# Optimization experiments

Measured on AMD Instinct MI355X. Metric: run time of the kernel, lower is better.

The kernel has to match this reference:

```python
import jax, jax.numpy as jnp
import numpy as np

H = 512      # hidden_size
NH = 4       # num_heads (default)
D = H // NH  # head_dim = 128
B = 2
S = 256
PI = float(np.pi)


def setup_inputs() -> dict:
    key = jax.random.key(0)
    ks = iter(jax.random.split(key, 40))
    n = lambda *s: jax.random.normal(next(ks), s, jnp.float32) * 0.02
    z = lambda *s: jnp.zeros(s, jnp.float32)
    return dict(
        x=jax.random.normal(next(ks), (B, S, H), jnp.float32),
        # WaveInteractionAttention projections (stored as (in,out): y = x @ W + b)
        Wq=n(H, H), bq=z(H), Wk=n(H, H), bk=z(H), Wv=n(H, H), bv=z(H), Wo=n(H, H), bo=z(H),
        # WaveletAttention Conv1d weights, torch layout (O, I, K), kernels 3/5/9
        cw1=n(H, H, 3), cb1=z(H), cw2=n(H, H, 5), cb2=z(H), cw3=n(H, H, 9), cb3=z(H),
        scale_w=jnp.ones((3,), jnp.float32) / 3.0, Wwl=n(H, H), bwl=z(H),
        # PhaseInteractionLayer
        Wtc=n(H, 2 * H), btc=z(2 * H), Wfc=n(2 * H, H), bfc=z(H),
        phase_shifts=jax.random.normal(next(ks), (1, 1, H), jnp.float32) * 0.1,
        # final concat projection + LayerNorm
        Wproj=n(3 * H, H), bproj=z(H), ln_g=jnp.ones((H,), jnp.float32), ln_b=z(H),
    )


def reference(x, Wq, bq, Wk, bk, Wv, bv, Wo, bo,
              cw1, cb1, cw2, cb2, cw3, cb3, scale_w, Wwl, bwl,
              Wtc, btc, Wfc, bfc, phase_shifts, Wproj, bproj, ln_g, ln_b):
    Bs, Sl, Hs = x.shape

    # ---- WaveInteractionAttention ----
    def heads(W, b):  # (B,S,H) -> (B,NH,S,D)
        return jnp.transpose((x @ W + b).reshape(Bs, Sl, NH, D), (0, 2, 1, 3))

    q, k, v = heads(Wq, bq), heads(Wk, bk), heads(Wv, bv)
    omega = jax.nn.sigmoid(q) * PI        # (B,NH,S,D)
    amp = jax.nn.sigmoid(k)
    ph = jnp.tanh(v) * PI
    pos = (jnp.arange(Sl)[:, None] - jnp.arange(Sl)[None, :]).astype(jnp.float32)  # (S,S): i-j
    # scores[b,h,i,j,d] = amp[b,h,i,d] * cos(omega[b,h,i,d]*(i-j) + phase[b,h,i,d])
    scores = amp[:, :, :, None, :] * jnp.cos(
        omega[:, :, :, None, :] * pos[None, None, :, :, None] + ph[:, :, :, None, :])
    patterns = jax.nn.softmax(scores * (1.0 / np.sqrt(D)), axis=3)  # softmax over j
    ctx = jnp.einsum('bhijd,bhjd->bhid', patterns, v)               # (B,NH,S,D)
    wave_out = jnp.transpose(ctx, (0, 2, 1, 3)).reshape(Bs, Sl, Hs) @ Wo + bo

    # ---- WaveletAttention (multi-scale Conv1d; 'same' length) ----
    xc = jnp.transpose(x, (0, 2, 1))  # (B,H,S)

    def conv(w, b, p):
        y = jax.lax.conv_general_dilated(xc, w, (1,), [(p, p)],
                                         dimension_numbers=('NCH', 'OIH', 'NCH'))
        return y + b[None, :, None]

    sw = jax.nn.softmax(scale_w)
    comb = sw[0] * conv(cw1, cb1, 1) + sw[1] * conv(cw2, cb2, 2) + sw[2] * conv(cw3, cb3, 4)
    wavelet_out = jnp.transpose(comb, (0, 2, 1)) @ Wwl + bwl

    # ---- PhaseInteractionLayer ----
    cr = x @ Wtc + btc
    real, imag = cr[..., :Hs], cr[..., Hs:]
    mag = jnp.sqrt(real ** 2 + imag ** 2 + 1e-5)
    p = jnp.arctan2(imag, real)  # (B,S,H)
    # mean_j cos(p_i - p_j + s) == cos(p_i+s)*mean_j cos(p_j) + sin(p_i+s)*mean_j sin(p_j)
    mc = jnp.mean(jnp.cos(p), axis=1, keepdims=True)
    ms = jnp.mean(jnp.sin(p), axis=1, keepdims=True)
    mixed = jnp.cos(p + phase_shifts) * mc + jnp.sin(p + phase_shifts) * ms
    new_p = p + 0.1 * mixed
    nc = jnp.concatenate([mag * jnp.cos(new_p), mag * jnp.sin(new_p)], axis=-1)
    phase_out = nc @ Wfc + bfc

    # ---- combine + residual + LayerNorm (dropout in eval mode = identity) ----
    combined = jnp.concatenate([wave_out, wavelet_out, phase_out], axis=-1) @ Wproj + bproj
    out = x + combined
    mu = jnp.mean(out, axis=-1, keepdims=True)
    var = jnp.mean((out - mu) ** 2, axis=-1, keepdims=True)
    return (out - mu) / jnp.sqrt(var + 1e-5) * ln_g + ln_b
```

## Files before the change

### kernel.cpp

```cpp
#include <hip/hip_runtime.h>
#include <math.h>

#define H 512
#define B 2
#define S 256
#define BS 512
#define PI_F 3.14159265358979323846f
#define INV_SQRT_D 0.08838834764831845f

typedef __attribute__((ext_vector_type(8))) short short8;
typedef __attribute__((ext_vector_type(4))) float f32x4;
typedef __attribute__((ext_vector_type(4))) unsigned short ushort4v;

__device__ __forceinline__ unsigned short f2bf(float f) {
    unsigned u = __float_as_uint(f);
    u += 0x7FFFu + ((u >> 16) & 1u);
    return (unsigned short)(u >> 16);
}
__device__ __forceinline__ float bf2f(unsigned short u) {
    return __uint_as_float((unsigned)u << 16);
}

__device__ __forceinline__ void softmax3(const float* sw, float& w0, float& w1, float& w2)
{
    float s0 = sw[0], s1 = sw[1], s2 = sw[2];
    float mx = fmaxf(s0, fmaxf(s1, s2));
    float e0 = __expf(s0 - mx), e1 = __expf(s1 - mx), e2 = __expf(s2 - mx);
    float inv = 1.f / (e0 + e1 + e2);
    w0 = e0 * inv; w1 = e1 * inv; w2 = e2 * inv;
}

__device__ __forceinline__ void gload16(const unsigned short* g, void* l) {
    __builtin_amdgcn_global_load_lds(
        (const __attribute__((address_space(1))) unsigned int*)g,
        (__attribute__((address_space(3))) unsigned int*)l,
        16, 0, 0);
}

template<int EPI>
__device__ __forceinline__ void gemm_body(
    const unsigned short* __restrict__ Ablk, int lda,
    const unsigned short* __restrict__ Btblk, int ldb,
    const float* __restrict__ bias,
    void* __restrict__ Cout, int ldc,
    int row0, int col0, int nk,
    unsigned short (*As)[4096], unsigned short (*Bs)[4096],
    unsigned short* __restrict__ aux = nullptr)
{
    const int tid = threadIdx.x;
    const int lane = tid & 63, wave = tid >> 6;
    const int wr = wave >> 1, wc = wave & 1;
    const int rowA = tid >> 3;
    const int sb = ((tid & 7) << 4) ^ ((rowA & 7) << 4);
    const size_t offA0 = (size_t)rowA * lda + (sb >> 1);
    const size_t offA1 = offA0 + (size_t)32 * lda;
    const size_t offB0 = (size_t)rowA * ldb + (sb >> 1);
    const size_t offB1 = offB0 + (size_t)32 * ldb;
    const unsigned ldsO0 = wave * 1024u, ldsO1 = ldsO0 + 4096u;

    const int fr = lane & 15, grp = lane >> 4;
    int aA[2][2], aB[2][2];
    #pragma unroll
    for (int kk = 0; kk < 2; ++kk)
        #pragma unroll
        for (int f = 0; f < 2; ++f) {
            int ra = wr * 32 + f * 16 + fr;
            int rb = wc * 32 + f * 16 + fr;
            aA[f][kk] = (ra * 128 + kk * 64 + grp * 16) ^ ((ra & 7) << 4);
            aB[f][kk] = (rb * 128 + kk * 64 + grp * 16) ^ ((rb & 7) << 4);
        }

    auto stage = [&](int buf, int k0) {
        char* ab = (char*)As[buf]; char* bb = (char*)Bs[buf];
        gload16(Ablk  + offA0 + k0, ab + ldsO0);
        gload16(Ablk  + offA1 + k0, ab + ldsO1);
        gload16(Btblk + offB0 + k0, bb + ldsO0);
        gload16(Btblk + offB1 + k0, bb + ldsO1);
    };

    stage(0, 0);
    __syncthreads();
    f32x4 acc[2][2] = {};
    int cur = 0;
    for (int t = 0; t < nk; ++t) {
        if (t + 1 < nk) stage(cur ^ 1, (t + 1) * 64);
        const char* AsB = (const char*)As[cur];
        const char* BsB = (const char*)Bs[cur];
        #pragma unroll
        for (int kk = 0; kk < 2; ++kk) {
            short8 a0 = *(const short8*)(AsB + aA[0][kk]);
            short8 a1 = *(const short8*)(AsB + aA[1][kk]);
            short8 b0 = *(const short8*)(BsB + aB[0][kk]);
            short8 b1 = *(const short8*)(BsB + aB[1][kk]);
            acc[0][0] = __builtin_amdgcn_mfma_f32_16x16x32_bf16(a0, b0, acc[0][0], 0, 0, 0);
            acc[0][1] = __builtin_amdgcn_mfma_f32_16x16x32_bf16(a0, b1, acc[0][1], 0, 0, 0);
            acc[1][0] = __builtin_amdgcn_mfma_f32_16x16x32_bf16(a1, b0, acc[1][0], 0, 0, 0);
            acc[1][1] = __builtin_amdgcn_mfma_f32_16x16x32_bf16(a1, b1, acc[1][1], 0, 0, 0);
        }
        __syncthreads();
        cur ^= 1;
    }

    const int erow = row0 + wr * 32 + grp * 4;
    const int ecol = col0 + wc * 32 + fr;
    #pragma unroll
    for (int fm = 0; fm < 2; ++fm)
        #pragma unroll
        for (int fn = 0; fn < 2; ++fn)
            #pragma unroll
            for (int j = 0; j < 4; ++j) {
                int r = erow + fm * 16 + j;
                int c = ecol + fn * 16;
                float v = acc[fm][fn][j];
                if (EPI == 1) {
                    v += bias[c];
                    if (c < 512)       v = PI_F / (1.f + __expf(-v));
                    else if (c < 1024) v = 1.f  / (1.f + __expf(-v));
                    ((float*)Cout)[(size_t)r * ldc + c] = v;
                    if (c >= 1024 && c < 1536)
                        aux[(size_t)r * 512 + (c - 1024)] = f2bf(v);
                } else if (EPI == 4) {
                    ((unsigned short*)Cout)[(size_t)r * ldc + c] = f2bf(v);
                } else {
                    ((float*)Cout)[(size_t)r * ldc + c] = v;
                }
            }
}

__device__ __forceinline__ void conv_body(
    const unsigned short* __restrict__ xpad,
    const unsigned short* __restrict__ WbigT,
    float* __restrict__ convP, int bm, int bn, int z,
    unsigned short (*As)[4096], unsigned short (*Bs)[4096])
{
    const int tid = threadIdx.x;
    const int lane = tid & 63, wave = tid >> 6;
    const int wr = wave >> 1, wc = wave & 1;
    const int rowA = tid >> 3;
    const int sb = ((tid & 7) << 4) ^ ((rowA & 7) << 4);
    const int sbk = sb >> 1;
    const int r0 = bm * 64 + rowA;
    const int base0 = ((r0 >> 8) * 264 + (r0 & 255)) * 512;
    const int r1 = r0 + 32;
    const int base1 = ((r1 >> 8) * 264 + (r1 & 255)) * 512;
    const size_t offB0 = (size_t)(bn * 64 + rowA) * 4608 + sbk;
    const size_t offB1 = offB0 + (size_t)32 * 4608;
    const unsigned ldsO0 = wave * 1024u, ldsO1 = ldsO0 + 4096u;
    const int kstart = z * 1152;

    const int fr = lane & 15, grp = lane >> 4;
    int aA[2][2], aB[2][2];
    #pragma unroll
    for (int kk = 0; kk < 2; ++kk)
        #pragma unroll
        for (int f = 0; f < 2; ++f) {
            int ra = wr * 32 + f * 16 + fr;
            int rb = wc * 32 + f * 16 + fr;
            aA[f][kk] = (ra * 128 + kk * 64 + grp * 16) ^ ((ra & 7) << 4);
            aB[f][kk] = (rb * 128 + kk * 64 + grp * 16) ^ ((rb & 7) << 4);
        }

    auto stage = [&](int buf, int k0) {
        int tap = k0 >> 9;
        int ro = tap * 512 + (k0 & 511) + sbk;
        char* ab = (char*)As[buf]; char* bb = (char*)Bs[buf];
        gload16(xpad + base0 + ro, ab + ldsO0);
        gload16(xpad + base1 + ro, ab + ldsO1);
        gload16(WbigT + offB0 + k0, bb + ldsO0);
        gload16(WbigT + offB1 + k0, bb + ldsO1);
    };

    stage(0, kstart);
    __syncthreads();
    f32x4 acc[2][2] = {};
    int cur = 0;
    for (int t = 0; t < 18; ++t) {
        if (t < 17) stage(cur ^ 1, kstart + (t + 1) * 64);
        const char* AsB = (const char*)As[cur];
        const char* BsB = (const char*)Bs[cur];
        #pragma unroll
        for (int kk = 0; kk < 2; ++kk) {
            short8 a0 = *(const short8*)(AsB + aA[0][kk]);
            short8 a1 = *(const short8*)(AsB + aA[1][kk]);
            short8 b0 = *(const short8*)(BsB + aB[0][kk]);
            short8 b1 = *(const short8*)(BsB + aB[1][kk]);
            acc[0][0] = __builtin_amdgcn_mfma_f32_16x16x32_bf16(a0, b0, acc[0][0], 0, 0, 0);
            acc[0][1] = __builtin_amdgcn_mfma_f32_16x16x32_bf16(a0, b1, acc[0][1], 0, 0, 0);
            acc[1][0] = __builtin_amdgcn_mfma_f32_16x16x32_bf16(a1, b0, acc[1][0], 0, 0, 0);
            acc[1][1] = __builtin_amdgcn_mfma_f32_16x16x32_bf16(a1, b1, acc[1][1], 0, 0, 0);
        }
        __syncthreads();
        cur ^= 1;
    }

    float* Cp = convP + (size_t)z * 262144;
    const int erow = bm * 64 + wr * 32 + grp * 4;
    const int ecol = bn * 64 + wc * 32 + fr;
    #pragma unroll
    for (int fm = 0; fm < 2; ++fm)
        #pragma unroll
        for (int fn = 0; fn < 2; ++fn)
            #pragma unroll
            for (int j = 0; j < 4; ++j)
                Cp[(size_t)(erow + fm * 16 + j) * 512 + ecol + fn * 16] = acc[fm][fn][j];
}

__global__ __launch_bounds__(256)
void prep_all(const float* __restrict__ x,
              const float* __restrict__ Wq, const float* __restrict__ Wk,
              const float* __restrict__ Wv, const float* __restrict__ Wtc,
              const float* __restrict__ Wo, const float* __restrict__ Wwl,
              const float* __restrict__ Wfc, const float* __restrict__ Wproj,
              const float* __restrict__ cw1, const float* __restrict__ cw2,
              const float* __restrict__ cw3, const float* __restrict__ scale_w,
              const float* __restrict__ bq, const float* __restrict__ bk,
              const float* __restrict__ bv, const float* __restrict__ btc,
              const float* __restrict__ cb1, const float* __restrict__ cb2,
              const float* __restrict__ cb3,
              const float* __restrict__ bo, const float* __restrict__ bwl,
              const float* __restrict__ bfc, const float* __restrict__ phase_shifts,
              unsigned short* __restrict__ xpad, unsigned short* __restrict__ WcatT,
              unsigned short* __restrict__ WbigT, unsigned short* __restrict__ WprojT,
              unsigned short* __restrict__ Wo_b, unsigned short* __restrict__ Wwl_b,
              unsigned short* __restrict__ Wfc_b,
              float* __restrict__ bcat1, float* __restrict__ beff,
              float* __restrict__ cps, float* __restrict__ sps,
              float* __restrict__ bias_effP)
{
    int bid = blockIdx.x, tid = threadIdx.x;

    if (bid < 64) {
        int k0 = bid * 24;
        float a0 = 0.f, a1 = 0.f;
        #pragma unroll
        for (int m = 0; m < 24; ++m) {
            int k = k0 + m;
            float w = (k < 512) ? bo[k] : (k < 1024) ? bwl[k - 512] : bfc[k - 1024];
            a0 = fmaf(w, Wproj[(size_t)k * 512 + tid], a0);
            a1 = fmaf(w, Wproj[(size_t)k * 512 + tid + 256], a1);
        }
        bias_effP[(size_t)bid * 512 + tid] = a0;
        bias_effP[(size_t)bid * 512 + tid + 256] = a1;
        return;
    }
    bid -= 64;
    if (bid < 1024) {
        int oi = bid * 256 + tid;
        int o = oi >> 9, i = oi & 511;
        float w0, w1, w2; softmax3(scale_w, w0, w1, w2);
        float wt[9];
        #pragma unroll
        for (int t = 0; t < 9; ++t) wt[t] = w2 * cw3[(size_t)oi * 9 + t];
        #pragma unroll
        for (int t = 0; t < 3; ++t) wt[t + 3] = fmaf(w0, cw1[(size_t)oi * 3 + t], wt[t + 3]);
        #pragma unroll
        for (int t = 0; t < 5; ++t) wt[t + 2] = fmaf(w1, cw2[(size_t)oi * 5 + t], wt[t + 2]);
        unsigned short* dst = WbigT + (size_t)o * 4608 + i;
        #pragma unroll
        for (int t = 0; t < 9; ++t) dst[t * 512] = f2bf(wt[t]);
        return;
    }
    bid -= 1024;
    if (bid < 2048) {
        __shared__ float tile[32][33];
        int t = bid;
        const float* src; unsigned short* dst;
        int srcld, dstld, ntk, drow0;
        if (t < 256)       {            src = Wq;    srcld = 512;  dst = WcatT;  dstld = 512;  ntk = 16; drow0 = 0; }
        else if (t < 512)  { t -= 256;  src = Wk;    srcld = 512;  dst = WcatT;  dstld = 512;  ntk = 16; drow0 = 512; }
        else if (t < 768)  { t -= 512;  src = Wv;    srcld = 512;  dst = WcatT;  dstld = 512;  ntk = 16; drow0 = 1024; }
        else if (t < 1280) { t -= 768;  src = Wtc;   srcld = 1024; dst = WcatT;  dstld = 512;  ntk = 16; drow0 = 1536; }
        else               { t -= 1280; src = Wproj; srcld = 512;  dst = WprojT; dstld = 1536; ntk = 48; drow0 = 0; }
        int tk = t % ntk, tn = t / ntk;
        int r8 = tid >> 5, c = tid & 31;
        #pragma unroll
        for (int rr = 0; rr < 4; ++rr) {
            int r = r8 + rr * 8;
            tile[r][c] = src[(size_t)(tk * 32 + r) * srcld + tn * 32 + c];
        }
        __syncthreads();
        #pragma unroll
        for (int rr = 0; rr < 4; ++rr) {
            int r = r8 + rr * 8;
            dst[(size_t)(drow0 + tn * 32 + r) * dstld + tk * 32 + c] = f2bf(tile[c][r]);
        }
        return;
    }
    bid -= 2048;
    if (bid < 264) {
        int e = bid * 1024 + tid * 4;
        int b = e / 135168, rem = e - b * 135168;
        int srow = rem >> 9, i4 = rem & 511;
        int s2 = srow - 4;
        ushort4v pk = {0, 0, 0, 0};
        if (s2 >= 0 && s2 < 256) {
            f32x4 v = *(const f32x4*)&x[((size_t)(b * 256 + s2) << 9) + i4];
            pk[0] = f2bf(v[0]); pk[1] = f2bf(v[1]); pk[2] = f2bf(v[2]); pk[3] = f2bf(v[3]);
        }
        *(ushort4v*)&xpad[e] = pk;
        return;
    }
    bid -= 264;
    if (bid < 1024) {
        int f = bid * 1024 + tid * 4;
        const float* src; unsigned short* dst; int o;
        if (f < 262144)      { src = Wo;  dst = Wo_b;  o = f; }
        else if (f < 524288) { src = Wwl; dst = Wwl_b; o = f - 262144; }
        else                 { src = Wfc; dst = Wfc_b; o = f - 524288; }
        f32x4 v = *(const f32x4*)&src[o];
        ushort4v pk;
        pk[0] = f2bf(v[0]); pk[1] = f2bf(v[1]); pk[2] = f2bf(v[2]); pk[3] = f2bf(v[3]);
        *(ushort4v*)&dst[o] = pk;
        return;
    }
    bid -= 1024;
    {
        int idx = bid * 256 + tid;
        if (idx < 2560) {
            float v;
            if (idx < 512)       v = bq[idx];
            else if (idx < 1024) v = bk[idx - 512];
            else if (idx < 1536) v = bv[idx - 1024];
            else                 v = btc[idx - 1536];
            bcat1[idx] = v;
        } else if (idx < 3072) {
            int c = idx - 2560;
            float w0, w1, w2; softmax3(scale_w, w0, w1, w2);
            beff[c] = w0 * cb1[c] + w1 * cb2[c] + w2 * cb3[c];
        } else if (idx < 3584) {
            int c = idx - 3072;
            float sn, cn; sincosf(phase_shifts[c], &sn, &cn);
            cps[c] = cn; sps[c] = sn;
        }
    }
}

__global__ __launch_bounds__(256)
void big_gemms(const unsigned short* __restrict__ xpad,
               const unsigned short* __restrict__ WbigT, float* __restrict__ convP,
               const unsigned short* __restrict__ WcatT, const float* __restrict__ bcat1,
               float* __restrict__ qkvt, unsigned short* __restrict__ vb16,
               const unsigned short* __restrict__ WprojT,
               const unsigned short* __restrict__ Wo_b, const unsigned short* __restrict__ Wwl_b,
               const unsigned short* __restrict__ Wfc_b,
               unsigned short* __restrict__ WeffCat_T)
{
    __shared__ unsigned short As[2][4096], Bs[2][4096];
    int bid = blockIdx.x;
    if (bid < 256) {
        conv_body(xpad, WbigT, convP, (bid >> 3) & 7, bid & 7, bid >> 6, As, Bs);
        return;
    }
    bid -= 256;
    if (bid < 320) {
        int bm = bid / 40, bn = bid % 40;
        int r0 = bm * 64;
        const unsigned short* Axp = xpad + ((size_t)(r0 >> 8) * 264 + (r0 & 255) + 4) * 512;
        gemm_body<1>(Axp, 512, WcatT + (size_t)bn * 64 * 512, 512, bcat1,
                     qkvt, 2560, r0, bn * 64, 8, As, Bs, vb16);
        return;
    }
    bid -= 320;
    if (bid < 64) {
        int bm = bid >> 3, bn = bid & 7;
        gemm_body<4>(WprojT + (size_t)bm * 64 * 1536, 1536, Wo_b + (size_t)bn * 64 * 512, 512,
                     nullptr, WeffCat_T, 2048, bm * 64, bn * 64, 8, As, Bs);
        return;
    }
    bid -= 64;
    if (bid < 64) {
        int bm = bid >> 3, bn = bid & 7;
        gemm_body<4>(WprojT + 512 + (size_t)bm * 64 * 1536, 1536, Wwl_b + (size_t)bn * 64 * 512, 512,
                     nullptr, WeffCat_T + 512, 2048, bm * 64, bn * 64, 8, As, Bs);
        return;
    }
    bid -= 64;
    {
        int bm = bid >> 4, bn = bid & 15;
        gemm_body<4>(WprojT + 1024 + (size_t)bm * 64 * 1536, 1536, Wfc_b + (size_t)bn * 64 * 512, 512,
                     nullptr, WeffCat_T + 1024, 2048, bm * 64, bn * 64, 8, As, Bs);
    }
}

__global__ __launch_bounds__(256)
void branches(const float* __restrict__ qkvt, const unsigned short* __restrict__ vb16,
              const float* __restrict__ cps, const float* __restrict__ sps,
              const float* __restrict__ convP, const float* __restrict__ beff,
              const float* __restrict__ bias_effP, const float* __restrict__ bproj,
              unsigned short* __restrict__ A_cat, float* __restrict__ bias_eff)
{
    int bid = blockIdx.x, tid = threadIdx.x;
    if (bid < 1024) {
        const int bi = bid >> 1;
        const int b = bi >> 8, i = bi & 255;
        const int c = ((bid & 1) << 8) + tid;
        const float* qrow = qkvt + (size_t)bi * 2560;
        const float om = qrow[c];
        const float am = qrow[512 + c] * INV_SQRT_D;
        const float ph = tanhf(qrow[1024 + c]) * PI_F;
        float cosom, sinom, cc, ss;
        sincosf(om, &sinom, &cosom);
        sincosf(fmaf(om, (float)i, ph), &ss, &cc);
        const unsigned short* vb = vb16 + (size_t)(b * 256) * 512 + c;
        float se = 0.f, sev = 0.f;
        #pragma unroll 4
        for (int j = 0; j < 256; ++j) {
            float e = __expf(am * cc);
            se += e;
            sev = fmaf(e, bf2f(vb[(size_t)j * 512]), sev);
            float cn = fmaf(cc, cosom, ss * sinom);
            ss = fmaf(ss, cosom, -cc * sinom);
            cc = cn;
        }
        A_cat[(size_t)bi * 2048 + c] = f2bf(sev / se);
        return;
    }
    bid -= 1024;
    if (bid < 1024) {
        const int b = bid >> 9, c = bid & 511;
        const int s = tid;
        const float* row = qkvt + (size_t)(b * 256 + s) * 2560 + 1536;
        float re = row[c], im = row[c + 512];
        float hyp2 = fmaf(re, re, im * im);
        float mag = sqrtf(hyp2 + 1e-5f);
        float rh = rsqrtf(fmaxf(hyp2, 1e-30f));
        float cp = re * rh, sp = im * rh;
        float cs = cp, sn = sp;
        #pragma unroll
        for (int m = 32; m; m >>= 1) { cs += __shfl_xor(cs, m); sn += __shfl_xor(sn, m); }
        __shared__ float wred[8];
        int w = s >> 6, l = s & 63;
        if (l == 0) { wred[w] = cs; wred[4 + w] = sn; }
        __syncthreads();
        float mcv = (wred[0] + wred[1] + wred[2] + wred[3]) * (1.f / 256.f);
        float msv = (wred[4] + wred[5] + wred[6] + wred[7]) * (1.f / 256.f);
        float cq = cps[c], sq = sps[c];
        float cpps = cp * cq - sp * sq;
        float spps = sp * cq + cp * sq;
        float d = 0.1f * (cpps * mcv + spps * msv);
        float d2 = d * d;
        float cosd = 1.f - d2 * (0.5f - d2 * (1.f / 24.f));
        float sind = d * (1.f - d2 * ((1.f / 6.f) - d2 * (1.f / 120.f)));
        float cnp = cp * cosd - sp * sind;
        float snp = sp * cosd + cp * sind;
        size_t o = (size_t)(b * 256 + s) * 2048 + c;
        A_cat[o + 1024] = f2bf(mag * cnp);
        A_cat[o + 1536] = f2bf(mag * snp);
        return;
    }
    bid -= 1024;
    if (bid < 1024) {
        int idx = bid * 256 + tid;
        int r = idx >> 9, c = idx & 511;
        float v = beff[c] + convP[idx] + convP[idx + 262144] + convP[idx + 524288] + convP[idx + 786432];
        A_cat[(size_t)r * 2048 + 512 + c] = f2bf(v);
        return;
    }
    bid -= 1024;
    {
        int j = bid * 256 + tid;
        float acc = bproj[j];
        #pragma unroll
        for (int p = 0; p < 64; ++p) acc += bias_effP[(size_t)p * 512 + j];
        bias_eff[j] = acc;
    }
}

__global__ __launch_bounds__(256)
void mid_gemm(const unsigned short* __restrict__ A_cat,
              const unsigned short* __restrict__ WeffCat_T,
              float* __restrict__ P)
{
    __shared__ unsigned short As[2][4096], Bs[2][4096];
    int bid = blockIdx.x;
    int z = bid >> 6, bm = (bid >> 3) & 7, bn = bid & 7;
    gemm_body<3>(A_cat + (size_t)bm * 64 * 2048 + z * 512, 2048,
                 WeffCat_T + (size_t)bn * 64 * 2048 + z * 512, 2048,
                 nullptr, P + (size_t)z * 262144, 512, bm * 64, bn * 64, 8, As, Bs);
}

__global__ __launch_bounds__(256)
void final_ln(const float* __restrict__ x, const float* __restrict__ P,
              const float* __restrict__ bias_eff,
              const float* __restrict__ g, const float* __restrict__ bta,
              float* __restrict__ out)
{
    int r = blockIdx.x, t = threadIdx.x;
    size_t o0 = (size_t)r * 512 + t, o1 = o0 + 256;
    float c0 = bias_eff[t]       + P[o0] + P[o0 + 262144] + P[o0 + 524288] + P[o0 + 786432];
    float c1 = bias_eff[t + 256] + P[o1] + P[o1 + 262144] + P[o1 + 524288] + P[o1 + 786432];
    float v0 = x[o0] + c0, v1 = x[o1] + c1;
    float sum = v0 + v1;
    #pragma unroll
    for (int m = 32; m; m >>= 1) sum += __shfl_xor(sum, m);
    __shared__ float wred[8];
    int w = t >> 6, l = t & 63;
    if (l == 0) wred[w] = sum;
    __syncthreads();
    float mu = (wred[0] + wred[1] + wred[2] + wred[3]) * (1.f / 512.f);
    float d0 = v0 - mu, d1 = v1 - mu;
    float s2 = d0 * d0 + d1 * d1;
    #pragma unroll
    for (int m = 32; m; m >>= 1) s2 += __shfl_xor(s2, m);
    if (l == 0) wred[4 + w] = s2;
    __syncthreads();
    float inv = rsqrtf((wred[4] + wred[5] + wred[6] + wred[7]) * (1.f / 512.f) + 1e-5f);
    out[o0] = d0 * inv * g[t]       + bta[t];
    out[o1] = d1 * inv * g[t + 256] + bta[t + 256];
}

extern "C" void kernel_launch(void* const* d_in, const int* in_sizes, int n_in,
                              void* d_out, int out_size, void* d_ws, size_t ws_size,
                              hipStream_t stream)
{
    const float* x   = (const float*)d_in[0];
    const float* Wq  = (const float*)d_in[1];
    const float* bq  = (const float*)d_in[2];
    const float* Wk  = (const float*)d_in[3];
    const float* bk  = (const float*)d_in[4];
    const float* Wv  = (const float*)d_in[5];
    const float* bv  = (const float*)d_in[6];
    const float* Wo  = (const float*)d_in[7];
    const float* bo  = (const float*)d_in[8];
    const float* cw1 = (const float*)d_in[9];
    const float* cb1 = (const float*)d_in[10];
    const float* cw2 = (const float*)d_in[11];
    const float* cb2 = (const float*)d_in[12];
    const float* cw3 = (const float*)d_in[13];
    const float* cb3 = (const float*)d_in[14];
    const float* scale_w = (const float*)d_in[15];
    const float* Wwl = (const float*)d_in[16];
    const float* bwl = (const float*)d_in[17];
    const float* Wtc = (const float*)d_in[18];
    const float* btc = (const float*)d_in[19];
    const float* Wfc = (const float*)d_in[20];
    const float* bfc = (const float*)d_in[21];
    const float* phase_shifts = (const float*)d_in[22];
    const float* Wproj = (const float*)d_in[23];
    const float* bproj = (const float*)d_in[24];
    const float* ln_g = (const float*)d_in[25];
    const float* ln_b = (const float*)d_in[26];
    float* out = (float*)d_out;

    float* wsf       = (float*)d_ws;
    float* qkvt      = wsf;
    float* convP     = qkvt + 1310720;
    float* P         = convP + 1048576;
    float* bias_effP = P + 1048576;
    float* bias_eff  = bias_effP + 32768;
    float* bcat1     = bias_eff + 512;
    float* beff      = bcat1 + 2560;
    float* cps       = beff + 512;
    float* sps       = cps + 512;
    unsigned short* u = (unsigned short*)(sps + 512);
    unsigned short* xpad     = u;
    unsigned short* WcatT    = xpad + 270336;
    unsigned short* WbigT    = WcatT + 1310720;
    unsigned short* WprojT   = WbigT + 2359296;
    unsigned short* Wo_b     = WprojT + 786432;
    unsigned short* Wwl_b    = Wo_b + 262144;
    unsigned short* Wfc_b    = Wwl_b + 262144;
    unsigned short* WeffCat_T= Wfc_b + 524288;
    unsigned short* A_cat    = WeffCat_T + 1048576;
    unsigned short* vb16     = A_cat + 1048576;

    prep_all<<<4438, 256, 0, stream>>>(x, Wq, Wk, Wv, Wtc, Wo, Wwl, Wfc, Wproj,
                                       cw1, cw2, cw3, scale_w,
                                       bq, bk, bv, btc, cb1, cb2, cb3,
                                       bo, bwl, bfc, phase_shifts,
                                       xpad, WcatT, WbigT, WprojT,
                                       Wo_b, Wwl_b, Wfc_b,
                                       bcat1, beff, cps, sps, bias_effP);

    big_gemms<<<832, 256, 0, stream>>>(xpad, WbigT, convP, WcatT, bcat1, qkvt, vb16,
                                       WprojT, Wo_b, Wwl_b, Wfc_b, WeffCat_T);

    branches<<<3074, 256, 0, stream>>>(qkvt, vb16, cps, sps, convP, beff,
                                       bias_effP, bproj, A_cat, bias_eff);

    mid_gemm<<<256, 256, 0, stream>>>(A_cat, WeffCat_T, P);

    final_ln<<<512, 256, 0, stream>>>(x, P, bias_eff, ln_g, ln_b, out);
}
```

Baseline: 64.03 us.

## Double conv split-K to 8 slices and fuse LayerNorm into mid GEMM via last-block counter

The conv GEMM's K range is split into 8 slices of 576 instead of 4 of 1152, doubling the conv blocks to 512 for better occupancy at the cost of extra partial-sum traffic in the reduction. The final LayerNorm kernel is removed. Its work, including the bias_eff reduction, moves into mid_gemm_ln, where an atomic per-row-tile counter lets the last of 32 blocks finish each 64-row tile. The branches kernel resets the counters. This saves one launch, but it serialises the LayerNorm onto only 8 blocks and adds fences and atomics.

After: 107.9 us. 68.5% more time.

```diff
diff --git a/kernel.cpp b/kernel.cpp
--- a/kernel.cpp
+++ b/kernel.cpp
@@ -146,7 +146,7 @@
     const size_t offB0 = (size_t)(bn * 64 + rowA) * 4608 + sbk;
     const size_t offB1 = offB0 + (size_t)32 * 4608;
     const unsigned ldsO0 = wave * 1024u, ldsO1 = ldsO0 + 4096u;
-    const int kstart = z * 1152;
+    const int kstart = z * 576;
 
     const int fr = lane & 15, grp = lane >> 4;
     int aA[2][2], aB[2][2];
@@ -174,8 +174,8 @@
     __syncthreads();
     f32x4 acc[2][2] = {};
     int cur = 0;
-    for (int t = 0; t < 18; ++t) {
-        if (t < 17) stage(cur ^ 1, kstart + (t + 1) * 64);
+    for (int t = 0; t < 9; ++t) {
+        if (t < 8) stage(cur ^ 1, kstart + (t + 1) * 64);
         const char* AsB = (const char*)As[cur];
         const char* BsB = (const char*)Bs[cur];
         #pragma unroll
@@ -347,11 +347,11 @@
 {
     __shared__ unsigned short As[2][4096], Bs[2][4096];
     int bid = blockIdx.x;
-    if (bid < 256) {
+    if (bid < 512) {
         conv_body(xpad, WbigT, convP, (bid >> 3) & 7, bid & 7, bid >> 6, As, Bs);
         return;
     }
-    bid -= 256;
+    bid -= 512;
     if (bid < 320) {
         int bm = bid / 40, bn = bid % 40;
         int r0 = bm * 64;
@@ -386,8 +386,7 @@
 void branches(const float* __restrict__ qkvt, const unsigned short* __restrict__ vb16,
               const float* __restrict__ cps, const float* __restrict__ sps,
               const float* __restrict__ convP, const float* __restrict__ beff,
-              const float* __restrict__ bias_effP, const float* __restrict__ bproj,
-              unsigned short* __restrict__ A_cat, float* __restrict__ bias_eff)
+              unsigned short* __restrict__ A_cat, int* __restrict__ cnt)
 {
     int bid = blockIdx.x, tid = threadIdx.x;
     if (bid < 1024) {
@@ -452,24 +451,23 @@
     if (bid < 1024) {
         int idx = bid * 256 + tid;
         int r = idx >> 9, c = idx & 511;
-        float v = beff[c] + convP[idx] + convP[idx + 262144] + convP[idx + 524288] + convP[idx + 786432];
+        float v = beff[c];
+        #pragma unroll
+        for (int z = 0; z < 8; ++z) v += convP[idx + (size_t)z * 262144];
         A_cat[(size_t)r * 2048 + 512 + c] = f2bf(v);
         return;
     }
-    bid -= 1024;
-    {
-        int j = bid * 256 + tid;
-        float acc = bproj[j];
-        #pragma unroll
-        for (int p = 0; p < 64; ++p) acc += bias_effP[(size_t)p * 512 + j];
-        bias_eff[j] = acc;
-    }
+    if (tid < 8) cnt[tid] = 0;
 }
 
 __global__ __launch_bounds__(256)
-void mid_gemm(const unsigned short* __restrict__ A_cat,
-              const unsigned short* __restrict__ WeffCat_T,
-              float* __restrict__ P)
+void mid_gemm_ln(const unsigned short* __restrict__ A_cat,
+                 const unsigned short* __restrict__ WeffCat_T,
+                 float* __restrict__ P, int* __restrict__ cnt,
+                 const float* __restrict__ x, const float* __restrict__ bias_effP,
+                 const float* __restrict__ bproj,
+                 const float* __restrict__ g, const float* __restrict__ bta,
+                 float* __restrict__ out)
 {
     __shared__ unsigned short As[2][4096], Bs[2][4096];
     int bid = blockIdx.x;
@@ -477,36 +475,51 @@
     gemm_body<3>(A_cat + (size_t)bm * 64 * 2048 + z * 512, 2048,
                  WeffCat_T + (size_t)bn * 64 * 2048 + z * 512, 2048,
                  nullptr, P + (size_t)z * 262144, 512, bm * 64, bn * 64, 8, As, Bs);
-}
-
-__global__ __launch_bounds__(256)
-void final_ln(const float* __restrict__ x, const float* __restrict__ P,
-              const float* __restrict__ bias_eff,
-              const float* __restrict__ g, const float* __restrict__ bta,
-              float* __restrict__ out)
-{
-    int r = blockIdx.x, t = threadIdx.x;
-    size_t o0 = (size_t)r * 512 + t, o1 = o0 + 256;
-    float c0 = bias_eff[t]       + P[o0] + P[o0 + 262144] + P[o0 + 524288] + P[o0 + 786432];
-    float c1 = bias_eff[t + 256] + P[o1] + P[o1 + 262144] + P[o1 + 524288] + P[o1 + 786432];
-    float v0 = x[o0] + c0, v1 = x[o1] + c1;
-    float sum = v0 + v1;
-    #pragma unroll
-    for (int m = 32; m; m >>= 1) sum += __shfl_xor(sum, m);
-    __shared__ float wred[8];
-    int w = t >> 6, l = t & 63;
-    if (l == 0) wred[w] = sum;
+
+    __threadfence();
+    __shared__ int lastFlag;
+    int tid = threadIdx.x;
+    if (tid == 0) lastFlag = (atomicAdd(&cnt[bm], 1) == 31);
     __syncthreads();
-    float mu = (wred[0] + wred[1] + wred[2] + wred[3]) * (1.f / 512.f);
-    float d0 = v0 - mu, d1 = v1 - mu;
-    float s2 = d0 * d0 + d1 * d1;
-    #pragma unroll
-    for (int m = 32; m; m >>= 1) s2 += __shfl_xor(s2, m);
-    if (l == 0) wred[4 + w] = s2;
+    if (!lastFlag) return;
+    __threadfence();
+
+    __shared__ float lds_bias[512], lds_g[512], lds_bt[512];
+    for (int c = tid; c < 512; c += 256) {
+        float acc = bproj[c];
+        #pragma unroll
+        for (int p = 0; p < 64; ++p) acc += bias_effP[(size_t)p * 512 + c];
+        lds_bias[c] = acc;
+        lds_g[c] = g[c];
+        lds_bt[c] = bta[c];
+    }
     __syncthreads();
-    float inv = rsqrtf((wred[4] + wred[5] + wred[6] + wred[7]) * (1.f / 512.f) + 1e-5f);
-    out[o0] = d0 * inv * g[t]       + bta[t];
-    out[o1] = d1 * inv * g[t + 256] + bta[t + 256];
+
+    int wave = tid >> 6, lane = tid & 63;
+    for (int rr = 0; rr < 16; ++rr) {
+        int r = bm * 64 + wave * 16 + rr;
+        float v[8];
+        float sum = 0.f, sq = 0.f;
+        #pragma unroll
+        for (int u8 = 0; u8 < 8; ++u8) {
+            int c = lane + u8 * 64;
+            size_t o = (size_t)r * 512 + c;
+            float val = x[o] + lds_bias[c] + P[o] + P[o + 262144] + P[o + 524288] + P[o + 786432];
+            v[u8] = val;
+            sum += val;
+            sq = fmaf(val, val, sq);
+        }
+        #pragma unroll
+        for (int m = 32; m; m >>= 1) { sum += __shfl_xor(sum, m); sq += __shfl_xor(sq, m); }
+        float mu = sum * (1.f / 512.f);
+        float var = sq * (1.f / 512.f) - mu * mu;
+        float inv = rsqrtf(var + 1e-5f);
+        #pragma unroll
+        for (int u8 = 0; u8 < 8; ++u8) {
+            int c = lane + u8 * 64;
+            out[(size_t)r * 512 + c] = (v[u8] - mu) * inv * lds_g[c] + lds_bt[c];
+        }
+    }
 }
 
 extern "C" void kernel_launch(void* const* d_in, const int* in_sizes, int n_in,
@@ -545,14 +558,14 @@
     float* wsf       = (float*)d_ws;
     float* qkvt      = wsf;
     float* convP     = qkvt + 1310720;
-    float* P         = convP + 1048576;
+    float* P         = convP + 2097152;
     float* bias_effP = P + 1048576;
-    float* bias_eff  = bias_effP + 32768;
-    float* bcat1     = bias_eff + 512;
+    float* bcat1     = bias_effP + 32768;
     float* beff      = bcat1 + 2560;
     float* cps       = beff + 512;
     float* sps       = cps + 512;
-    unsigned short* u = (unsigned short*)(sps + 512);
+    int*   cnt       = (int*)(sps + 512);
+    unsigned short* u = (unsigned short*)(cnt + 128);
     unsigned short* xpad     = u;
     unsigned short* WcatT    = xpad + 270336;
     unsigned short* WbigT    = WcatT + 1310720;
@@ -572,13 +585,11 @@
                                        Wo_b, Wwl_b, Wfc_b,
                                        bcat1, beff, cps, sps, bias_effP);
 
-    big_gemms<<<832, 256, 0, stream>>>(xpad, WbigT, convP, WcatT, bcat1, qkvt, vb16,
-                                       WprojT, Wo_b, Wwl_b, Wfc_b, WeffCat_T);
-
-    branches<<<3074, 256, 0, stream>>>(qkvt, vb16, cps, sps, convP, beff,
-                                       bias_effP, bproj, A_cat, bias_eff);
-
-    mid_gemm<<<256, 256, 0, stream>>>(A_cat, WeffCat_T, P);
-
-    final_ln<<<512, 256, 0, stream>>>(x, P, bias_eff, ln_g, ln_b, out);
-}
+    big_gemms<<<1088, 256, 0, stream>>>(xpad, WbigT, convP, WcatT, bcat1, qkvt, vb16,
+                                        WprojT, Wo_b, Wwl_b, Wfc_b, WeffCat_T);
+
+    branches<<<3073, 256, 0, stream>>>(qkvt, vb16, cps, sps, convP, beff, A_cat, cnt);
+
+    mid_gemm_ln<<<256, 256, 0, stream>>>(A_cat, WeffCat_T, P, cnt,
+                                         x, bias_effP, bproj, ln_g, ln_b, out);
+}
```
